# Optimization experiments

Hardware: AMD Instinct MI355X
Metric: run time of the kernel (lower is better)

## Reference

```python
import jax, jax.numpy as jnp
import numpy as np

EPS = 1e-8  # torch F.cosine_similarity eps


def _wn(v, g):
    # torch weight_norm: w = g * v / ||v|| (norm per output channel, over input dim)
    return g[:, None] * v / jnp.linalg.norm(v, axis=1, keepdims=True)


def setup_inputs() -> dict:
    key = jax.random.key(0)
    ks = jax.random.split(key, 8)
    N, C, L = 4, 512, 4096     # batch, input channels, flattened spatial/time
    D, K = 256, 8192           # code channels, num codes
    x = jax.random.normal(ks[0], (N, C, L), jnp.float32)
    in_v = jax.random.normal(ks[1], (D, C), jnp.float32) / np.sqrt(C).astype(np.float32)
    in_g = jnp.linalg.norm(in_v, axis=1)            # weight_norm init: g = ||v||
    in_b = (jax.random.uniform(ks[2], (D,), jnp.float32) - 0.5) / np.sqrt(C).astype(np.float32)
    out_v = jax.random.normal(ks[3], (C, D), jnp.float32) / np.sqrt(D).astype(np.float32)
    out_g = jnp.linalg.norm(out_v, axis=1)
    out_b = (jax.random.uniform(ks[4], (C,), jnp.float32) - 0.5) / np.sqrt(D).astype(np.float32)
    codebook = jax.random.normal(ks[5], (K, D), jnp.float32)
    return {"x": x, "in_v": in_v, "in_g": in_g, "in_b": in_b,
            "out_v": out_v, "out_g": out_g, "out_b": out_b, "codebook": codebook}


def reference(x, in_v, in_g, in_b, out_v, out_g, out_b, codebook):
    # input 1x1 conv (pointwise linear over channels)
    W_in = _wn(in_v, in_g)                                   # (D, C)
    z_e = jnp.einsum('ncl,dc->ndl', x, W_in) + in_b[None, :, None]  # (N, D, L)

    # cosine-similarity codebook search
    ze_t = z_e.transpose(0, 2, 1)                            # (N, L, D)
    ze_n = ze_t / jnp.maximum(jnp.linalg.norm(ze_t, axis=-1, keepdims=True), EPS)
    cb_n = codebook / jnp.maximum(jnp.linalg.norm(codebook, axis=-1, keepdims=True), EPS)
    sim = jnp.einsum('nld,kd->nlk', ze_n, cb_n)              # (N, L, K) large intermediate
    code_index = jnp.argmax(sim, axis=-1)                    # (N, L) int
    z_q = codebook[code_index].transpose(0, 2, 1)            # (N, D, L)

    # per-sample VQ losses
    cb_loss = jnp.mean((z_q - jax.lax.stop_gradient(z_e)) ** 2, axis=(1, 2))
    cm_loss = jnp.mean((z_e - jax.lax.stop_gradient(z_q)) ** 2, axis=(1, 2))

    # straight-through estimator (training mode); numerically equal to z_q
    z_q_st = jax.lax.stop_gradient(z_q) + (z_e - jax.lax.stop_gradient(z_e))

    # output 1x1 conv
    W_out = _wn(out_v, out_g)                                # (C, D)
    y = jnp.einsum('ndl,cd->ncl', z_q_st, W_out) + out_b[None, :, None]  # (N, C, L)
    return y, code_index, cb_loss, cm_loss
```

## Files before the change

kernel.cpp:

```cpp
#include <hip/hip_runtime.h>
#include <math.h>

#define N_ 4
#define C_ 512
#define L_ 4096
#define D_ 256
#define K_ 8192
#define NL_ 16384

#define OUT_IDX_OFF (N_*C_*L_)
#define OUT_CB_OFF  (OUT_IDX_OFF + NL_)

#define WS_ZT   0
#define WS_P    (WS_ZT + (size_t)NL_*D_)
#define WS_Z2   (WS_P + (size_t)K_*C_)
#define WS_CB2  (WS_Z2 + (size_t)NL_*D_)
#define WS_PART (WS_CB2 + (size_t)K_*D_)
#define WS_WIN  (WS_PART + (size_t)NL_*64*4)
#define WS_WOUT (WS_WIN + (size_t)D_*C_)
#define WS_INVN (WS_WOUT + (size_t)C_*D_)
#define WS_IDX  (WS_INVN + (size_t)K_)
#define WS_LOSS (WS_IDX + (size_t)NL_)

typedef __bf16 bf16x8 __attribute__((ext_vector_type(8)));
typedef float  f32x4  __attribute__((ext_vector_type(4)));
typedef unsigned int u32;

__device__ __forceinline__ unsigned short f2bf(float f) {
    u32 u = __float_as_uint(f);
    u32 r = (u + 0x7fffu + ((u >> 16) & 1u)) >> 16;
    return (unsigned short)r;
}
__device__ __forceinline__ float bf2f(unsigned short h) {
    return __uint_as_float(((u32)h) << 16);
}

__device__ __forceinline__ float waveReduceSum64(float s) {
    #pragma unroll
    for (int off = 32; off; off >>= 1) s += __shfl_xor(s, off, 64);
    return s;
}

__device__ __forceinline__ bool pref(float av, int ai, float bv, int bi) {
    return (av > bv) || (av == bv && ai < bi);
}
__device__ __forceinline__ void push2(float& v1, int& i1, float& v2, int& i2,
                                      float wv, int wi) {
    if (pref(wv, wi, v1, i1)) { v2 = v1; i2 = i1; v1 = wv; i1 = wi; }
    else if (pref(wv, wi, v2, i2)) { v2 = wv; i2 = wi; }
}

__global__ __launch_bounds__(64) void prep_kernel(
    const float* __restrict__ in_v, const float* __restrict__ in_g,
    const float* __restrict__ out_v, const float* __restrict__ out_g,
    float* __restrict__ Win, float* __restrict__ Wout,
    float* __restrict__ lossacc)
{
    const int b = blockIdx.x;
    const int t = threadIdx.x;
    if (b == 0 && t < N_) lossacc[t] = 0.0f;
    if (b < D_) {
        const float* v = in_v + (size_t)b * C_;
        float4 a0 = *(const float4*)(v + t * 4);
        float4 a1 = *(const float4*)(v + 256 + t * 4);
        float s = a0.x*a0.x + a0.y*a0.y + a0.z*a0.z + a0.w*a0.w
                + a1.x*a1.x + a1.y*a1.y + a1.z*a1.z + a1.w*a1.w;
        s = waveReduceSum64(s);
        float scale = in_g[b] / sqrtf(s);
        float* w = Win + (size_t)b * C_;
        float4 o0, o1;
        o0.x=a0.x*scale; o0.y=a0.y*scale; o0.z=a0.z*scale; o0.w=a0.w*scale;
        o1.x=a1.x*scale; o1.y=a1.y*scale; o1.z=a1.z*scale; o1.w=a1.w*scale;
        *(float4*)(w + t*4) = o0;
        *(float4*)(w + 256 + t*4) = o1;
    } else {
        const int r = b - D_;
        const float* v = out_v + (size_t)r * D_;
        float4 a0 = *(const float4*)(v + t * 4);
        float s = a0.x*a0.x + a0.y*a0.y + a0.z*a0.z + a0.w*a0.w;
        s = waveReduceSum64(s);
        float scale = out_g[r] / sqrtf(s);
        float4 o0;
        o0.x=a0.x*scale; o0.y=a0.y*scale; o0.z=a0.z*scale; o0.w=a0.w*scale;
        *(float4*)(Wout + (size_t)r * D_ + t*4) = o0;
    }
}

__global__ __launch_bounds__(64) void cb2_kernel(
    const float* __restrict__ cb, float* __restrict__ invn)
{
    const int k = blockIdx.x;
    const int t = threadIdx.x;
    float4 v = *(const float4*)(cb + (size_t)k * D_ + t * 4);
    float s = v.x*v.x + v.y*v.y + v.z*v.z + v.w*v.w;
    s = waveReduceSum64(s);
    if (t == 0) invn[k] = 1.0f / fmaxf(sqrtf(s), 1e-8f);
}

__global__ __launch_bounds__(256) void cb2f_kernel(
    const float* __restrict__ cb, const float* __restrict__ invn,
    unsigned short* __restrict__ CB2F)
{
    const int c16 = blockIdx.x;
    const int t = threadIdx.x;
    const int kc = t >> 4, nl = t & 15;
    const int code = c16 * 16 + nl;
    const float inv = invn[code];
    const float* src = cb + (size_t)code * D_ + (kc & 7) * 32;
    unsigned short* dst = CB2F + ((size_t)(c16 * 16 + kc) * 64) * 8;
    #pragma unroll
    for (int lh = 0; lh < 4; ++lh) {
        float4 x0 = *(const float4*)(src + lh * 8);
        float4 x1 = *(const float4*)(src + lh * 8 + 4);
        float f[8] = {x0.x, x0.y, x0.z, x0.w, x1.x, x1.y, x1.z, x1.w};
        unsigned short o[8];
        #pragma unroll
        for (int j = 0; j < 8; ++j) {
            float v = f[j] * inv;
            unsigned short h = f2bf(v);
            o[j] = (kc < 8) ? h : f2bf(v - bf2f(h));
        }
        unsigned short* dp = dst + (lh * 16 + nl) * 8;
        *(ushort4*)&dp[0] = make_ushort4(o[0], o[1], o[2], o[3]);
        *(ushort4*)&dp[4] = make_ushort4(o[4], o[5], o[6], o[7]);
    }
}

__global__ __launch_bounds__(256) void ze_kernel(
    const float* __restrict__ x, const float* __restrict__ Win,
    const float* __restrict__ inb, float* __restrict__ Zt,
    unsigned short* __restrict__ Z2)
{
    __shared__ float Al[2][16][64];
    __shared__ float Bl[2][16][68];
    const int tid = threadIdx.x;
    const int ty = tid >> 4, tx = tid & 15;
    const int l0 = blockIdx.x * 64;
    const int d0 = blockIdx.y * 64;
    const int n  = blockIdx.z;
    const float* xn = x + (size_t)n * C_ * L_;

    const int ac = tid >> 4, alq = tid & 15;
    const int bd = tid >> 2, bq  = tid & 3;

    float acc[4][4];
    #pragma unroll
    for (int i = 0; i < 4; ++i)
        #pragma unroll
        for (int j = 0; j < 4; ++j) acc[i][j] = 0.0f;

    auto stage = [&](int cc, int buf) {
        float4 av = *(const float4*)(xn + (size_t)(cc*16 + ac) * L_ + l0 + alq*4);
        *(float4*)&Al[buf][ac][alq*4] = av;
        float4 bv = *(const float4*)(Win + (size_t)(d0 + bd) * C_ + cc*16 + bq*4);
        Bl[buf][bq*4+0][bd] = bv.x; Bl[buf][bq*4+1][bd] = bv.y;
        Bl[buf][bq*4+2][bd] = bv.z; Bl[buf][bq*4+3][bd] = bv.w;
    };

    stage(0, 0);
    for (int cc = 0; cc < 32; ++cc) {
        __syncthreads();
        if (cc + 1 < 32) stage(cc + 1, (cc + 1) & 1);
        const int buf = cc & 1;
        #pragma unroll
        for (int k = 0; k < 16; ++k) {
            float4 a = *(const float4*)&Al[buf][k][ty*4];
            float4 b = *(const float4*)&Bl[buf][k][tx*4];
            acc[0][0]=fmaf(a.x,b.x,acc[0][0]); acc[0][1]=fmaf(a.x,b.y,acc[0][1]);
            acc[0][2]=fmaf(a.x,b.z,acc[0][2]); acc[0][3]=fmaf(a.x,b.w,acc[0][3]);
            acc[1][0]=fmaf(a.y,b.x,acc[1][0]); acc[1][1]=fmaf(a.y,b.y,acc[1][1]);
            acc[1][2]=fmaf(a.y,b.z,acc[1][2]); acc[1][3]=fmaf(a.y,b.w,acc[1][3]);
            acc[2][0]=fmaf(a.z,b.x,acc[2][0]); acc[2][1]=fmaf(a.z,b.y,acc[2][1]);
            acc[2][2]=fmaf(a.z,b.z,acc[2][2]); acc[2][3]=fmaf(a.z,b.w,acc[2][3]);
            acc[3][0]=fmaf(a.w,b.x,acc[3][0]); acc[3][1]=fmaf(a.w,b.y,acc[3][1]);
            acc[3][2]=fmaf(a.w,b.z,acc[3][2]); acc[3][3]=fmaf(a.w,b.w,acc[3][3]);
        }
    }
    float4 bias = *(const float4*)(inb + d0 + tx*4);
    #pragma unroll
    for (int i = 0; i < 4; ++i) {
        float4 o;
        o.x = acc[i][0] + bias.x; o.y = acc[i][1] + bias.y;
        o.z = acc[i][2] + bias.z; o.w = acc[i][3] + bias.w;
        const size_t row = (size_t)(n*L_ + l0 + ty*4 + i);
        *(float4*)&Zt[row * D_ + d0 + tx*4] = o;
        ushort4 h, lo;
        h.x = f2bf(o.x); h.y = f2bf(o.y); h.z = f2bf(o.z); h.w = f2bf(o.w);
        lo.x = f2bf(o.x - bf2f(h.x)); lo.y = f2bf(o.y - bf2f(h.y));
        lo.z = f2bf(o.z - bf2f(h.z)); lo.w = f2bf(o.w - bf2f(h.w));
        *(ushort4*)&Z2[row * 512 + d0 + tx*4]       = h;
        *(ushort4*)&Z2[row * 512 + 256 + d0 + tx*4] = lo;
    }
}

__global__ __launch_bounds__(256) void pmat_kernel(
    const float* __restrict__ cb, const float* __restrict__ Wout,
    float* __restrict__ P)
{
    __shared__ float Al[2][16][68];
    __shared__ float Bl[2][16][68];
    const int tid = threadIdx.x;
    const int ty = tid >> 4, tx = tid & 15;
    const int k0 = blockIdx.x * 64;
    const int c0 = blockIdx.y * 64;
    const int ar = tid >> 2, aq = tid & 3;

    float acc[4][4];
    #pragma unroll
    for (int i = 0; i < 4; ++i)
        #pragma unroll
        for (int j = 0; j < 4; ++j) acc[i][j] = 0.0f;

    auto stage = [&](int dc, int buf) {
        float4 av = *(const float4*)(cb + (size_t)(k0 + ar) * D_ + dc*16 + aq*4);
        Al[buf][aq*4+0][ar] = av.x; Al[buf][aq*4+1][ar] = av.y;
        Al[buf][aq*4+2][ar] = av.z; Al[buf][aq*4+3][ar] = av.w;
        float4 bv = *(const float4*)(Wout + (size_t)(c0 + ar) * D_ + dc*16 + aq*4);
        Bl[buf][aq*4+0][ar] = bv.x; Bl[buf][aq*4+1][ar] = bv.y;
        Bl[buf][aq*4+2][ar] = bv.z; Bl[buf][aq*4+3][ar] = bv.w;
    };

    stage(0, 0);
    for (int dc = 0; dc < 16; ++dc) {
        __syncthreads();
        if (dc + 1 < 16) stage(dc + 1, (dc + 1) & 1);
        const int buf = dc & 1;
        #pragma unroll
        for (int k = 0; k < 16; ++k) {
            float4 a = *(const float4*)&Al[buf][k][ty*4];
            float4 b = *(const float4*)&Bl[buf][k][tx*4];
            acc[0][0]=fmaf(a.x,b.x,acc[0][0]); acc[0][1]=fmaf(a.x,b.y,acc[0][1]);
            acc[0][2]=fmaf(a.x,b.z,acc[0][2]); acc[0][3]=fmaf(a.x,b.w,acc[0][3]);
            acc[1][0]=fmaf(a.y,b.x,acc[1][0]); acc[1][1]=fmaf(a.y,b.y,acc[1][1]);
            acc[1][2]=fmaf(a.y,b.z,acc[1][2]); acc[1][3]=fmaf(a.y,b.w,acc[1][3]);
            acc[2][0]=fmaf(a.z,b.x,acc[2][0]); acc[2][1]=fmaf(a.z,b.y,acc[2][1]);
            acc[2][2]=fmaf(a.z,b.z,acc[2][2]); acc[2][3]=fmaf(a.z,b.w,acc[2][3]);
            acc[3][0]=fmaf(a.w,b.x,acc[3][0]); acc[3][1]=fmaf(a.w,b.y,acc[3][1]);
            acc[3][2]=fmaf(a.w,b.z,acc[3][2]); acc[3][3]=fmaf(a.w,b.w,acc[3][3]);
        }
    }
    #pragma unroll
    for (int i = 0; i < 4; ++i) {
        float4 o;
        o.x = acc[i][0]; o.y = acc[i][1]; o.z = acc[i][2]; o.w = acc[i][3];
        *(float4*)&P[(size_t)(k0 + ty*4 + i) * C_ + c0 + tx*4] = o;
    }
}

__global__ __launch_bounds__(256, 2) void sim_kernel(
    const unsigned short* __restrict__ Z2, const unsigned short* __restrict__ CB2F,
    float* __restrict__ Part)
{
    const int tid = threadIdx.x;
    const int w = tid >> 6, l = tid & 63;
    const int bid = blockIdx.x;
    const int ks    = bid & 3;
    const int mtile = bid >> 2;
    const int m0 = mtile * 64 + w * 16;
    const int n0 = ks * 2048;

    const char* Abase = (const char*)Z2 + (size_t)(m0 + (l & 15)) * 1024
                        + ((l >> 4) * 16);
    bf16x8 af[16];
    #pragma unroll
    for (int f = 0; f < 8; ++f) {
        af[f]     = *(const bf16x8*)(Abase + f * 64);
        af[f + 8] = *(const bf16x8*)(Abase + 512 + f * 64);
    }

    const char* Bbase = (const char*)CB2F + (size_t)(n0 >> 4) * 16384 + l * 16;

    float bv1[4], bv2[4]; int bi1[4], bi2[4];
    #pragma unroll
    for (int t = 0; t < 4; ++t) {
        bv1[t] = -3.0e38f; bv2[t] = -3.0e38f;
        bi1[t] = 0x7FFFFFFF; bi2[t] = 0x7FFFFFFF;
    }

    for (int c = 0; c < 128; ++c) {
        const char* p = Bbase + (size_t)c * 16384;
        bf16x8 bg[16];
        #pragma unroll
        for (int f = 0; f < 16; ++f)
            bg[f] = *(const bf16x8*)(p + f * 1024);

        f32x4 a0 = {0.f,0.f,0.f,0.f}, a1 = a0, a2 = a0, a3 = a0;
        #pragma unroll
        for (int f = 0; f < 8; f += 2) {
            a0 = __builtin_amdgcn_mfma_f32_16x16x32_bf16(af[f],   bg[f],   a0, 0,0,0);
            a1 = __builtin_amdgcn_mfma_f32_16x16x32_bf16(af[f+1], bg[f+1], a1, 0,0,0);
            a2 = __builtin_amdgcn_mfma_f32_16x16x32_bf16(af[f+8], bg[f],   a2, 0,0,0);
            a3 = __builtin_amdgcn_mfma_f32_16x16x32_bf16(af[f+9], bg[f+1], a3, 0,0,0);
            a0 = __builtin_amdgcn_mfma_f32_16x16x32_bf16(af[f],   bg[f+8], a0, 0,0,0);
            a1 = __builtin_amdgcn_mfma_f32_16x16x32_bf16(af[f+1], bg[f+9], a1, 0,0,0);
        }
        f32x4 s01 = a0 + a1, s23 = a2 + a3;
        f32x4 s = s01 + s23;

        const int colbase = n0 + c * 16 + (l & 15);
        #pragma unroll
        for (int t = 0; t < 4; ++t)
            push2(bv1[t], bi1[t], bv2[t], bi2[t], s[t], colbase);
    }

    #pragma unroll
    for (int t = 0; t < 4; ++t) {
        float v1 = bv1[t], v2 = bv2[t];
        int   i1 = bi1[t], i2 = bi2[t];
        #pragma unroll
        for (int mask = 1; mask < 16; mask <<= 1) {
            float ov1 = __shfl_xor(v1, mask, 64);
            int   oi1 = __shfl_xor(i1, mask, 64);
            float ov2 = __shfl_xor(v2, mask, 64);
            int   oi2 = __shfl_xor(i2, mask, 64);
            push2(v1, i1, v2, i2, ov1, oi1);
            push2(v1, i1, v2, i2, ov2, oi2);
        }
        if ((l & 15) == 0) {
            const int row = m0 + (l >> 4) * 4 + t;
            float4 o;
            o.x = v1; o.y = __int_as_float(i1);
            o.z = v2; o.w = __int_as_float(i2);
            *(float4*)&Part[((size_t)row * 4 + ks) * 4] = o;
        }
    }
}

__global__ __launch_bounds__(256) void argmax_kernel(
    const float* __restrict__ Part, const float* __restrict__ Zt,
    const float* __restrict__ cb, const float* __restrict__ invn,
    int* __restrict__ idxout, float* __restrict__ fidxout)
{
    const int w = threadIdx.x >> 6, l = threadIdx.x & 63;
    const int row = blockIdx.x * 4 + w;
    float v1 = -3.0e38f, v2 = -3.0e38f;
    int   i1 = 0x7FFFFFFF, i2 = 0x7FFFFFFF;
    if (l < 4) {
        float4 p = *(const float4*)&Part[((size_t)row * 4 + l) * 4];
        v1 = p.x; i1 = __float_as_int(p.y);
        v2 = p.z; i2 = __float_as_int(p.w);
    }
    #pragma unroll
    for (int mask = 1; mask < 4; mask <<= 1) {
        float ov1 = __shfl_xor(v1, mask, 64);
        int   oi1 = __shfl_xor(i1, mask, 64);
        float ov2 = __shfl_xor(v2, mask, 64);
        int   oi2 = __shfl_xor(i2, mask, 64);
        push2(v1, i1, v2, i2, ov1, oi1);
        push2(v1, i1, v2, i2, ov2, oi2);
    }
    v1 = __shfl(v1, 0, 64); i1 = __shfl(i1, 0, 64);
    v2 = __shfl(v2, 0, 64); i2 = __shfl(i2, 0, 64);
    const float* z  = Zt + (size_t)row * D_;
    float4 zv = *(const float4*)(z + l*4);
    float4 a  = *(const float4*)(cb + (size_t)i1 * D_ + l*4);
    float4 b  = *(const float4*)(cb + (size_t)i2 * D_ + l*4);
    float s1 = zv.x*a.x + zv.y*a.y + zv.z*a.z + zv.w*a.w;
    float s2 = zv.x*b.x + zv.y*b.y + zv.z*b.z + zv.w*b.w;
    s1 = waveReduceSum64(s1);
    s2 = waveReduceSum64(s2);
    float e1 = s1 * invn[i1];
    float e2 = s2 * invn[i2];
    int win = (e2 > e1 || (e2 == e1 && i2 < i1)) ? i2 : i1;
    if (l == 0) { idxout[row] = win; fidxout[row] = (float)win; }
}

__global__ __launch_bounds__(256) void loss_kernel(
    const float* __restrict__ Zt, const float* __restrict__ cb,
    const int* __restrict__ idx, float* __restrict__ lossacc)
{
    __shared__ float red[4];
    const int tid = threadIdx.x;
    const int r = blockIdx.x * 64 + (tid >> 2);
    const int q = tid & 3;
    const int n = r >> 12;
    const int code = idx[r];
    const float* zp = Zt + (size_t)r * D_ + q * 64;
    const float* cp = cb + (size_t)code * D_ + q * 64;
    float s = 0.0f;
    #pragma unroll
    for (int it = 0; it < 16; ++it) {
        float4 a = *(const float4*)(zp + it*4);
        float4 c = *(const float4*)(cp + it*4);
        float dx = c.x - a.x, dy = c.y - a.y, dz = c.z - a.z, dw = c.w - a.w;
        s += dx*dx + dy*dy + dz*dz + dw*dw;
    }
    s = waveReduceSum64(s);
    if ((tid & 63) == 0) red[tid >> 6] = s;
    __syncthreads();
    if (tid == 0) atomicAdd(&lossacc[n], red[0] + red[1] + red[2] + red[3]);
}

__global__ __launch_bounds__(256) void y_kernel(
    const float* __restrict__ P, const int* __restrict__ idx,
    const float* __restrict__ outb, float* __restrict__ y)
{
    __shared__ float bias[128];
    const int t = threadIdx.x;
    const int c0 = blockIdx.y * 128;
    const int n = blockIdx.z;
    const int l = blockIdx.x * 256 + t;
    if (t < 128) bias[t] = outb[c0 + t];
    __syncthreads();
    const int code = idx[n * L_ + l];
    const float* prow = P + (size_t)code * C_ + c0;
    float* yb = y + ((size_t)n * C_ + c0) * L_ + l;
    #pragma unroll 4
    for (int c = 0; c < 128; ++c) {
        yb[(size_t)c * L_] = prow[c] + bias[c];
    }
}

__global__ __launch_bounds__(64) void fin_kernel(
    const float* __restrict__ lossacc, float* __restrict__ out)
{
    const int t = threadIdx.x;
    if (t < 8) out[t] = lossacc[t & 3] * (1.0f / (float)(D_ * L_));
}

extern "C" void kernel_launch(void* const* d_in, const int* in_sizes, int n_in,
                              void* d_out, int out_size, void* d_ws, size_t ws_size,
                              hipStream_t stream) {
    (void)in_sizes; (void)n_in; (void)out_size; (void)ws_size;
    const float* x     = (const float*)d_in[0];
    const float* in_v  = (const float*)d_in[1];
    const float* in_g  = (const float*)d_in[2];
    const float* in_b  = (const float*)d_in[3];
    const float* out_v = (const float*)d_in[4];
    const float* out_g = (const float*)d_in[5];
    const float* out_b = (const float*)d_in[6];
    const float* cb    = (const float*)d_in[7];
    float* out = (float*)d_out;
    float* ws  = (float*)d_ws;

    float*          Zt     = ws + WS_ZT;
    float*          P      = ws + WS_P;
    unsigned short* Z2     = (unsigned short*)(ws + WS_Z2);
    unsigned short* CB2F   = (unsigned short*)(ws + WS_CB2);
    float*          Part   = ws + WS_PART;
    float*          Win    = ws + WS_WIN;
    float*          Wout   = ws + WS_WOUT;
    float*          invn   = ws + WS_INVN;
    int*            idx    = (int*)(ws + WS_IDX);
    float*          lossac = ws + WS_LOSS;

    prep_kernel<<<dim3(D_ + C_), 64, 0, stream>>>(in_v, in_g, out_v, out_g,
                                                  Win, Wout, lossac);
    cb2_kernel<<<dim3(K_), 64, 0, stream>>>(cb, invn);
    cb2f_kernel<<<dim3(512), 256, 0, stream>>>(cb, invn, CB2F);
    ze_kernel<<<dim3(64, 4, 4), 256, 0, stream>>>(x, Win, in_b, Zt, Z2);
    pmat_kernel<<<dim3(128, 8), 256, 0, stream>>>(cb, Wout, P);
    sim_kernel<<<dim3(1024), 256, 0, stream>>>(Z2, CB2F, Part);
    argmax_kernel<<<dim3(4096), 256, 0, stream>>>(Part, Zt, cb, invn,
                                                  idx, out + OUT_IDX_OFF);
    loss_kernel<<<dim3(256), 256, 0, stream>>>(Zt, cb, idx, lossac);
    y_kernel<<<dim3(16, 4, 4), 256, 0, stream>>>(P, idx, out_b, out);
    fin_kernel<<<dim3(1), 64, 0, stream>>>(lossac, out + OUT_CB_OFF);
}
```

Baseline: 750.6 us.

## Double rows per wave in sim kernel to reuse codebook fragments

Each wave in the similarity GEMM now handles two 16-row A tiles (32 rows) instead of one, so every codebook B fragment loaded from global memory feeds twice as many MFMAs. The grid is halved to 512 blocks to match. The aim is to cut B-operand load traffic per FLOP. The cost is doubled A-fragment and top-2 tracking registers, which may lower occupancy under the launch bounds of 2 blocks, and fewer blocks leave less parallelism to spread across the CUs.

```diff
diff --git a/kernel.cpp b/kernel.cpp
--- a/kernel.cpp
+++ b/kernel.cpp
@@ -256,23 +256,26 @@
     const int bid = blockIdx.x;
     const int ks    = bid & 3;
     const int mtile = bid >> 2;
-    const int m0 = mtile * 64 + w * 16;
+    const int m0 = mtile * 128 + w * 32;
     const int n0 = ks * 2048;
 
-    const char* Abase = (const char*)Z2 + (size_t)(m0 + (l & 15)) * 1024
-                        + ((l >> 4) * 16);
-    bf16x8 af[16];
+    const char* Abase0 = (const char*)Z2 + (size_t)(m0 + (l & 15)) * 1024
+                         + ((l >> 4) * 16);
+    const char* Abase1 = Abase0 + 16 * 1024;
+    bf16x8 af0[16], af1[16];
     #pragma unroll
     for (int f = 0; f < 8; ++f) {
-        af[f]     = *(const bf16x8*)(Abase + f * 64);
-        af[f + 8] = *(const bf16x8*)(Abase + 512 + f * 64);
+        af0[f]     = *(const bf16x8*)(Abase0 + f * 64);
+        af0[f + 8] = *(const bf16x8*)(Abase0 + 512 + f * 64);
+        af1[f]     = *(const bf16x8*)(Abase1 + f * 64);
+        af1[f + 8] = *(const bf16x8*)(Abase1 + 512 + f * 64);
     }
 
     const char* Bbase = (const char*)CB2F + (size_t)(n0 >> 4) * 16384 + l * 16;
 
-    float bv1[4], bv2[4]; int bi1[4], bi2[4];
-    #pragma unroll
-    for (int t = 0; t < 4; ++t) {
+    float bv1[8], bv2[8]; int bi1[8], bi2[8];
+    #pragma unroll
+    for (int t = 0; t < 8; ++t) {
         bv1[t] = -3.0e38f; bv2[t] = -3.0e38f;
         bi1[t] = 0x7FFFFFFF; bi2[t] = 0x7FFFFFFF;
     }
@@ -284,29 +287,39 @@
         for (int f = 0; f < 16; ++f)
             bg[f] = *(const bf16x8*)(p + f * 1024);
 
-        f32x4 a0 = {0.f,0.f,0.f,0.f}, a1 = a0, a2 = a0, a3 = a0;
+        f32x4 x0 = {0.f,0.f,0.f,0.f}, x1 = x0, y0 = x0, y1 = x0;
         #pragma unroll
         for (int f = 0; f < 8; f += 2) {
-            a0 = __builtin_amdgcn_mfma_f32_16x16x32_bf16(af[f],   bg[f],   a0, 0,0,0);
-            a1 = __builtin_amdgcn_mfma_f32_16x16x32_bf16(af[f+1], bg[f+1], a1, 0,0,0);
-            a2 = __builtin_amdgcn_mfma_f32_16x16x32_bf16(af[f+8], bg[f],   a2, 0,0,0);
-            a3 = __builtin_amdgcn_mfma_f32_16x16x32_bf16(af[f+9], bg[f+1], a3, 0,0,0);
-            a0 = __builtin_amdgcn_mfma_f32_16x16x32_bf16(af[f],   bg[f+8], a0, 0,0,0);
-            a1 = __builtin_amdgcn_mfma_f32_16x16x32_bf16(af[f+1], bg[f+9], a1, 0,0,0);
-        }
-        f32x4 s01 = a0 + a1, s23 = a2 + a3;
-        f32x4 s = s01 + s23;
+            x0 = __builtin_amdgcn_mfma_f32_16x16x32_bf16(af0[f],   bg[f],   x0, 0,0,0);
+            x1 = __builtin_amdgcn_mfma_f32_16x16x32_bf16(af0[f+1], bg[f+1], x1, 0,0,0);
+            x0 = __builtin_amdgcn_mfma_f32_16x16x32_bf16(af0[f+8], bg[f],   x0, 0,0,0);
+            x1 = __builtin_amdgcn_mfma_f32_16x16x32_bf16(af0[f+9], bg[f+1], x1, 0,0,0);
+            y0 = __builtin_amdgcn_mfma_f32_16x16x32_bf16(af1[f],   bg[f],   y0, 0,0,0);
+            y1 = __builtin_amdgcn_mfma_f32_16x16x32_bf16(af1[f+1], bg[f+1], y1, 0,0,0);
+            y0 = __builtin_amdgcn_mfma_f32_16x16x32_bf16(af1[f+8], bg[f],   y0, 0,0,0);
+            y1 = __builtin_amdgcn_mfma_f32_16x16x32_bf16(af1[f+9], bg[f+1], y1, 0,0,0);
+        }
+        #pragma unroll
+        for (int f = 0; f < 8; f += 2) {
+            x0 = __builtin_amdgcn_mfma_f32_16x16x32_bf16(af0[f],   bg[f+8], x0, 0,0,0);
+            x1 = __builtin_amdgcn_mfma_f32_16x16x32_bf16(af0[f+1], bg[f+9], x1, 0,0,0);
+            y0 = __builtin_amdgcn_mfma_f32_16x16x32_bf16(af1[f],   bg[f+8], y0, 0,0,0);
+            y1 = __builtin_amdgcn_mfma_f32_16x16x32_bf16(af1[f+1], bg[f+9], y1, 0,0,0);
+        }
+        f32x4 s0 = x0 + x1, s1 = y0 + y1;
 
         const int colbase = n0 + c * 16 + (l & 15);
         #pragma unroll
-        for (int t = 0; t < 4; ++t)
-            push2(bv1[t], bi1[t], bv2[t], bi2[t], s[t], colbase);
-    }
-
-    #pragma unroll
-    for (int t = 0; t < 4; ++t) {
-        float v1 = bv1[t], v2 = bv2[t];
-        int   i1 = bi1[t], i2 = bi2[t];
+        for (int t = 0; t < 4; ++t) {
+            push2(bv1[t],   bi1[t],   bv2[t],   bi2[t],   s0[t], colbase);
+            push2(bv1[t+4], bi1[t+4], bv2[t+4], bi2[t+4], s1[t], colbase);
+        }
+    }
+
+    #pragma unroll
+    for (int tt = 0; tt < 8; ++tt) {
+        float v1 = bv1[tt], v2 = bv2[tt];
+        int   i1 = bi1[tt], i2 = bi2[tt];
         #pragma unroll
         for (int mask = 1; mask < 16; mask <<= 1) {
             float ov1 = __shfl_xor(v1, mask, 64);
@@ -317,7 +330,7 @@
             push2(v1, i1, v2, i2, ov2, oi2);
         }
         if ((l & 15) == 0) {
-            const int row = m0 + (l >> 4) * 4 + t;
+            const int row = m0 + (tt >> 2) * 16 + (l >> 4) * 4 + (tt & 3);
             float4 o;
             o.x = v1; o.y = __int_as_float(i1);
             o.z = v2; o.w = __int_as_float(i2);
@@ -450,7 +463,7 @@
     cb2f_kernel<<<dim3(512), 256, 0, stream>>>(cb, invn, CB2F);
     ze_kernel<<<dim3(64, 4, 4), 256, 0, stream>>>(x, Win, in_b, Zt, Z2);
     pmat_kernel<<<dim3(128, 8), 256, 0, stream>>>(cb, Wout, P);
-    sim_kernel<<<dim3(1024), 256, 0, stream>>>(Z2, CB2F, Part);
+    sim_kernel<<<dim3(512), 256, 0, stream>>>(Z2, CB2F, Part);
     argmax_kernel<<<dim3(4096), 256, 0, stream>>>(Part, Zt, cb, invn,
                                                   idx, out + OUT_IDX_OFF);
     loss_kernel<<<dim3(256), 256, 0, stream>>>(Zt, cb, idx, lossac);
```

After: 831.5 us. 10.8% more time.

## Stage codebook tiles in LDS via async global-to-LDS double buffering in sim kernel

Applied to the files above, without the earlier changes.

In the similarity kernel, the four waves now share codebook chunks. Each chunk is loaded once per block into a double-buffered LDS tile using global_load_lds, where before every wave loaded the B fragments from global memory itself. Each block also handles two M tiles in sequence, so the grid drops from 1024 to 512 blocks. The aim is to cut redundant global/L2 traffic for the codebook and overlap the next chunk's load with the current MFMAs. The cost is a __syncthreads per chunk, LDS reads, and fewer blocks in flight, which could reduce parallelism.

```diff
diff --git a/kernel.cpp b/kernel.cpp
--- a/kernel.cpp
+++ b/kernel.cpp
@@ -48,6 +48,13 @@
                                       float wv, int wi) {
     if (pref(wv, wi, v1, i1)) { v2 = v1; i2 = i1; v1 = wv; i1 = wi; }
     else if (pref(wv, wi, v2, i2)) { v2 = wv; i2 = wi; }
+}
+
+__device__ __forceinline__ void gload_lds16(const void* g, void* l) {
+    __builtin_amdgcn_global_load_lds(
+        (const __attribute__((address_space(1))) void*)g,
+        (__attribute__((address_space(3))) void*)l,
+        16, 0, 0);
 }
 
 __global__ __launch_bounds__(64) void prep_kernel(
@@ -251,77 +258,103 @@
     const unsigned short* __restrict__ Z2, const unsigned short* __restrict__ CB2F,
     float* __restrict__ Part)
 {
+    __shared__ char lds[2][16384];
     const int tid = threadIdx.x;
     const int w = tid >> 6, l = tid & 63;
     const int bid = blockIdx.x;
-    const int ks    = bid & 3;
-    const int mtile = bid >> 2;
-    const int m0 = mtile * 64 + w * 16;
+    const int ks = bid & 3;
     const int n0 = ks * 2048;
-
-    const char* Abase = (const char*)Z2 + (size_t)(m0 + (l & 15)) * 1024
-                        + ((l >> 4) * 16);
-    bf16x8 af[16];
-    #pragma unroll
-    for (int f = 0; f < 8; ++f) {
-        af[f]     = *(const bf16x8*)(Abase + f * 64);
-        af[f + 8] = *(const bf16x8*)(Abase + 512 + f * 64);
-    }
-
-    const char* Bbase = (const char*)CB2F + (size_t)(n0 >> 4) * 16384 + l * 16;
-
-    float bv1[4], bv2[4]; int bi1[4], bi2[4];
-    #pragma unroll
-    for (int t = 0; t < 4; ++t) {
-        bv1[t] = -3.0e38f; bv2[t] = -3.0e38f;
-        bi1[t] = 0x7FFFFFFF; bi2[t] = 0x7FFFFFFF;
-    }
-
-    for (int c = 0; c < 128; ++c) {
-        const char* p = Bbase + (size_t)c * 16384;
-        bf16x8 bg[16];
-        #pragma unroll
-        for (int f = 0; f < 16; ++f)
-            bg[f] = *(const bf16x8*)(p + f * 1024);
-
-        f32x4 a0 = {0.f,0.f,0.f,0.f}, a1 = a0, a2 = a0, a3 = a0;
-        #pragma unroll
-        for (int f = 0; f < 8; f += 2) {
-            a0 = __builtin_amdgcn_mfma_f32_16x16x32_bf16(af[f],   bg[f],   a0, 0,0,0);
-            a1 = __builtin_amdgcn_mfma_f32_16x16x32_bf16(af[f+1], bg[f+1], a1, 0,0,0);
-            a2 = __builtin_amdgcn_mfma_f32_16x16x32_bf16(af[f+8], bg[f],   a2, 0,0,0);
-            a3 = __builtin_amdgcn_mfma_f32_16x16x32_bf16(af[f+9], bg[f+1], a3, 0,0,0);
-            a0 = __builtin_amdgcn_mfma_f32_16x16x32_bf16(af[f],   bg[f+8], a0, 0,0,0);
-            a1 = __builtin_amdgcn_mfma_f32_16x16x32_bf16(af[f+1], bg[f+9], a1, 0,0,0);
-        }
-        f32x4 s01 = a0 + a1, s23 = a2 + a3;
-        f32x4 s = s01 + s23;
-
-        const int colbase = n0 + c * 16 + (l & 15);
-        #pragma unroll
-        for (int t = 0; t < 4; ++t)
-            push2(bv1[t], bi1[t], bv2[t], bi2[t], s[t], colbase);
-    }
-
-    #pragma unroll
-    for (int t = 0; t < 4; ++t) {
-        float v1 = bv1[t], v2 = bv2[t];
-        int   i1 = bi1[t], i2 = bi2[t];
-        #pragma unroll
-        for (int mask = 1; mask < 16; mask <<= 1) {
-            float ov1 = __shfl_xor(v1, mask, 64);
-            int   oi1 = __shfl_xor(i1, mask, 64);
-            float ov2 = __shfl_xor(v2, mask, 64);
-            int   oi2 = __shfl_xor(i2, mask, 64);
-            push2(v1, i1, v2, i2, ov1, oi1);
-            push2(v1, i1, v2, i2, ov2, oi2);
-        }
-        if ((l & 15) == 0) {
-            const int row = m0 + (l >> 4) * 4 + t;
-            float4 o;
-            o.x = v1; o.y = __int_as_float(i1);
-            o.z = v2; o.w = __int_as_float(i2);
-            *(float4*)&Part[((size_t)row * 4 + ks) * 4] = o;
+    const char* Bchunk = (const char*)CB2F + (size_t)(n0 >> 4) * 16384;
+
+    for (int rep = 0; rep < 2; ++rep) {
+        const int mtile = (bid >> 2) * 2 + rep;
+        const int m0 = mtile * 64 + w * 16;
+
+        const char* Abase = (const char*)Z2 + (size_t)(m0 + (l & 15)) * 1024
+                            + ((l >> 4) * 16);
+        bf16x8 af[16];
+        #pragma unroll
+        for (int f = 0; f < 8; ++f) {
+            af[f]     = *(const bf16x8*)(Abase + f * 64);
+            af[f + 8] = *(const bf16x8*)(Abase + 512 + f * 64);
+        }
+        asm volatile("" ::: "memory");
+
+        float bv1[4], bv2[4]; int bi1[4], bi2[4];
+        #pragma unroll
+        for (int t = 0; t < 4; ++t) {
+            bv1[t] = -3.0e38f; bv2[t] = -3.0e38f;
+            bi1[t] = 0x7FFFFFFF; bi2[t] = 0x7FFFFFFF;
+        }
+
+        {
+            const char* s = Bchunk + (size_t)w * 4096 + (size_t)l * 16;
+            char* d = &lds[0][w * 4096];
+            gload_lds16(s,        d);
+            gload_lds16(s + 1024, d + 1024);
+            gload_lds16(s + 2048, d + 2048);
+            gload_lds16(s + 3072, d + 3072);
+        }
+        __syncthreads();
+
+        for (int c = 0; c < 128; ++c) {
+            const int buf = c & 1;
+            if (c + 1 < 128) {
+                const char* s = Bchunk + (size_t)(c + 1) * 16384
+                                + (size_t)w * 4096 + (size_t)l * 16;
+                char* d = &lds[buf ^ 1][w * 4096];
+                gload_lds16(s,        d);
+                gload_lds16(s + 1024, d + 1024);
+                gload_lds16(s + 2048, d + 2048);
+                gload_lds16(s + 3072, d + 3072);
+            }
+            const char* p = &lds[buf][l * 16];
+            bf16x8 bg[16];
+            #pragma unroll
+            for (int f = 0; f < 16; ++f)
+                bg[f] = *(const bf16x8*)(p + (size_t)f * 1024);
+
+            f32x4 a0 = {0.f,0.f,0.f,0.f}, a1 = a0, a2 = a0, a3 = a0;
+            #pragma unroll
+            for (int f = 0; f < 8; f += 2) {
+                a0 = __builtin_amdgcn_mfma_f32_16x16x32_bf16(af[f],   bg[f],   a0, 0,0,0);
+                a1 = __builtin_amdgcn_mfma_f32_16x16x32_bf16(af[f+1], bg[f+1], a1, 0,0,0);
+                a2 = __builtin_amdgcn_mfma_f32_16x16x32_bf16(af[f+8], bg[f],   a2, 0,0,0);
+                a3 = __builtin_amdgcn_mfma_f32_16x16x32_bf16(af[f+9], bg[f+1], a3, 0,0,0);
+                a0 = __builtin_amdgcn_mfma_f32_16x16x32_bf16(af[f],   bg[f+8], a0, 0,0,0);
+                a1 = __builtin_amdgcn_mfma_f32_16x16x32_bf16(af[f+1], bg[f+9], a1, 0,0,0);
+            }
+            f32x4 s01 = a0 + a1, s23 = a2 + a3;
+            f32x4 s = s01 + s23;
+
+            const int colbase = n0 + c * 16 + (l & 15);
+            #pragma unroll
+            for (int t = 0; t < 4; ++t)
+                push2(bv1[t], bi1[t], bv2[t], bi2[t], s[t], colbase);
+
+            __syncthreads();
+        }
+
+        #pragma unroll
+        for (int t = 0; t < 4; ++t) {
+            float v1 = bv1[t], v2 = bv2[t];
+            int   i1 = bi1[t], i2 = bi2[t];
+            #pragma unroll
+            for (int mask = 1; mask < 16; mask <<= 1) {
+                float ov1 = __shfl_xor(v1, mask, 64);
+                int   oi1 = __shfl_xor(i1, mask, 64);
+                float ov2 = __shfl_xor(v2, mask, 64);
+                int   oi2 = __shfl_xor(i2, mask, 64);
+                push2(v1, i1, v2, i2, ov1, oi1);
+                push2(v1, i1, v2, i2, ov2, oi2);
+            }
+            if ((l & 15) == 0) {
+                const int row = m0 + (l >> 4) * 4 + t;
+                float4 o;
+                o.x = v1; o.y = __int_as_float(i1);
+                o.z = v2; o.w = __int_as_float(i2);
+                *(float4*)&Part[((size_t)row * 4 + ks) * 4] = o;
+            }
         }
     }
 }
@@ -450,7 +483,7 @@
     cb2f_kernel<<<dim3(512), 256, 0, stream>>>(cb, invn, CB2F);
     ze_kernel<<<dim3(64, 4, 4), 256, 0, stream>>>(x, Win, in_b, Zt, Z2);
     pmat_kernel<<<dim3(128, 8), 256, 0, stream>>>(cb, Wout, P);
-    sim_kernel<<<dim3(1024), 256, 0, stream>>>(Z2, CB2F, Part);
+    sim_kernel<<<dim3(512), 256, 0, stream>>>(Z2, CB2F, Part);
     argmax_kernel<<<dim3(4096), 256, 0, stream>>>(Part, Zt, cb, invn,
                                                   idx, out + OUT_IDX_OFF);
     loss_kernel<<<dim3(256), 256, 0, stream>>>(Zt, cb, idx, lossac);
```

After: 746.3 us. About the same (-0.6%).

## Stage codebook tiles into LDS via async global_load_lds with 4-deep pipeline

Applied to the files above, without the earlier changes.

The similarity kernel now copies each codebook chunk into shared memory with direct global-to-LDS loads, prefetched three chunks ahead in a 4-slot ring buffer. Each block loads a chunk once and shares it across its four waves, where before every wave read the same B data from global memory itself. Ordering relies on manual vmcnt waits plus a barrier per iteration. The cost is 64KB of LDS per block, which may lower occupancy below the launch-bound target of 2 blocks, and the hand-counted waits are fragile.

```diff
diff --git a/kernel.cpp b/kernel.cpp
--- a/kernel.cpp
+++ b/kernel.cpp
@@ -48,6 +48,13 @@
                                       float wv, int wi) {
     if (pref(wv, wi, v1, i1)) { v2 = v1; i2 = i1; v1 = wv; i1 = wi; }
     else if (pref(wv, wi, v2, i2)) { v2 = wv; i2 = wi; }
+}
+
+__device__ __forceinline__ void gload_lds16(const void* g, void* l) {
+    __builtin_amdgcn_global_load_lds(
+        (const __attribute__((address_space(1))) void*)g,
+        (__attribute__((address_space(3))) void*)l,
+        16, 0, 0);
 }
 
 __global__ __launch_bounds__(64) void prep_kernel(
@@ -251,13 +258,15 @@
     const unsigned short* __restrict__ Z2, const unsigned short* __restrict__ CB2F,
     float* __restrict__ Part)
 {
+    __shared__ char lds[4][16384];
     const int tid = threadIdx.x;
     const int w = tid >> 6, l = tid & 63;
     const int bid = blockIdx.x;
-    const int ks    = bid & 3;
+    const int ks = bid & 3;
     const int mtile = bid >> 2;
     const int m0 = mtile * 64 + w * 16;
     const int n0 = ks * 2048;
+    const char* Bchunk = (const char*)CB2F + (size_t)(n0 >> 4) * 16384;
 
     const char* Abase = (const char*)Z2 + (size_t)(m0 + (l & 15)) * 1024
                         + ((l >> 4) * 16);
@@ -267,8 +276,9 @@
         af[f]     = *(const bf16x8*)(Abase + f * 64);
         af[f + 8] = *(const bf16x8*)(Abase + 512 + f * 64);
     }
-
-    const char* Bbase = (const char*)CB2F + (size_t)(n0 >> 4) * 16384 + l * 16;
+    #pragma unroll
+    for (int f = 0; f < 16; ++f) asm volatile("" : "+v"(af[f]));
+    asm volatile("s_waitcnt vmcnt(0)" ::: "memory");
 
     float bv1[4], bv2[4]; int bi1[4], bi2[4];
     #pragma unroll
@@ -277,12 +287,30 @@
         bi1[t] = 0x7FFFFFFF; bi2[t] = 0x7FFFFFFF;
     }
 
+    auto stage = [&](int ch) {
+        const char* s = Bchunk + (size_t)ch * 16384 + (size_t)w * 4096
+                        + (size_t)l * 16;
+        char* d = &lds[ch & 3][w * 4096];
+        gload_lds16(s,        d);
+        gload_lds16(s + 1024, d + 1024);
+        gload_lds16(s + 2048, d + 2048);
+        gload_lds16(s + 3072, d + 3072);
+    };
+
+    stage(0); stage(1); stage(2);
+
     for (int c = 0; c < 128; ++c) {
-        const char* p = Bbase + (size_t)c * 16384;
+        if (c <= 125)      { asm volatile("s_waitcnt vmcnt(8)" ::: "memory"); }
+        else if (c == 126) { asm volatile("s_waitcnt vmcnt(4)" ::: "memory"); }
+        else               { asm volatile("s_waitcnt vmcnt(0)" ::: "memory"); }
+        __builtin_amdgcn_s_barrier();
+        if (c + 3 < 128) stage(c + 3);
+
+        const char* p = &lds[c & 3][l * 16];
         bf16x8 bg[16];
         #pragma unroll
         for (int f = 0; f < 16; ++f)
-            bg[f] = *(const bf16x8*)(p + f * 1024);
+            bg[f] = *(const bf16x8*)(p + (size_t)f * 1024);
 
         f32x4 a0 = {0.f,0.f,0.f,0.f}, a1 = a0, a2 = a0, a3 = a0;
         #pragma unroll
```

Result: no change. 752.9 us (+0.3%).
